# Kernel optimization log

Measured on AMD Instinct MI355X. Metric: run time of the kernel, lower is better.

## Reference

```python
import jax, jax.numpy as jnp
import numpy as np

D_MODEL = 512
N_HEAD = 8
D_HEAD = 64
N_LAYER = 4
D_INNER = 2048
IN_CH = 2048
N_CLS = 64
B, T = 2, 2048
LN_EPS = 1e-5


def layer_norm(x, s, b):
    mu = jnp.mean(x, axis=-1, keepdims=True)
    var = jnp.mean(jnp.square(x - mu), axis=-1, keepdims=True)
    return (x - mu) * jax.lax.rsqrt(var + LN_EPS) * s + b


def rel_shift(x):
    # x: [q, k, b, n] -> Transformer-XL relative shift
    q, k, b, n = x.shape
    zp = jnp.zeros((q, 1, b, n), x.dtype)
    x = jnp.concatenate([zp, x], axis=1)          # [q, k+1, b, n]
    x = x.reshape(k + 1, q, b, n)[1:]             # drop first row
    return x.reshape(q, k, b, n)


def setup_inputs() -> dict:
    key = jax.random.key(0)
    ks = jax.random.split(key, 12)
    s = 0.02
    return {
        "x": jax.random.normal(ks[0], (B, IN_CH, T), jnp.float32),
        "emb_w": jax.random.normal(ks[1], (D_MODEL, IN_CH), jnp.float32) * s,
        "emb_b": jnp.zeros((D_MODEL,), jnp.float32),
        "r_w_bias": jax.random.normal(ks[2], (N_HEAD, D_HEAD), jnp.float32) * s,
        "r_r_bias": jax.random.normal(ks[3], (N_HEAD, D_HEAD), jnp.float32) * s,
        "qkv_w": jax.random.normal(ks[4], (N_LAYER, 3 * N_HEAD * D_HEAD, D_MODEL), jnp.float32) * s,
        "qkv_b": jnp.zeros((N_LAYER, 3 * N_HEAD * D_HEAD), jnp.float32),
        "r_proj_w": jax.random.normal(ks[5], (N_LAYER, N_HEAD * D_HEAD, D_MODEL), jnp.float32) * s,
        "o_w": jax.random.normal(ks[6], (N_LAYER, D_MODEL, N_HEAD * D_HEAD), jnp.float32) * s,
        "ln1_s": jnp.ones((N_LAYER, D_MODEL), jnp.float32),
        "ln1_b": jnp.zeros((N_LAYER, D_MODEL), jnp.float32),
        "ff1_w": jax.random.normal(ks[7], (N_LAYER, D_INNER, D_MODEL), jnp.float32) * s,
        "ff1_b": jnp.zeros((N_LAYER, D_INNER), jnp.float32),
        "ff2_w": jax.random.normal(ks[8], (N_LAYER, D_MODEL, D_INNER), jnp.float32) * s,
        "ff2_b": jnp.zeros((N_LAYER, D_MODEL), jnp.float32),
        "ln2_s": jnp.ones((N_LAYER, D_MODEL), jnp.float32),
        "ln2_b": jnp.zeros((N_LAYER, D_MODEL), jnp.float32),
        "cls_w": jax.random.normal(ks[9], (N_CLS, D_MODEL), jnp.float32) * s,
        "cls_b": jnp.zeros((N_CLS,), jnp.float32),
    }


def reference(x, emb_w, emb_b, r_w_bias, r_r_bias, qkv_w, qkv_b, r_proj_w, o_w,
              ln1_s, ln1_b, ff1_w, ff1_b, ff2_w, ff2_b, ln2_s, ln2_b, cls_w, cls_b):
    b, _, t = x.shape
    d = D_MODEL
    # 1x1 conv embedding, then to [T, B, d_model] layout as in _forward
    h = jnp.einsum('dc,bct->tbd', emb_w, x) + emb_b

    # sinusoidal positional embedding over pos_seq = klen-1 .. 0 (klen == qlen, mem_len=0)
    pos_seq = jnp.arange(t - 1, -1, -1, dtype=h.dtype)
    inv_freq = 1.0 / (10000.0 ** (jnp.arange(0, d, 2, dtype=h.dtype) / d))
    sinusoid = pos_seq[:, None] * inv_freq[None, :]
    pos_emb = jnp.concatenate([jnp.sin(sinusoid), jnp.cos(sinusoid)], axis=-1)  # [T, d]

    scale = 1.0 / (D_HEAD ** 0.5)
    for i in range(N_LAYER):
        w = h
        heads = jnp.einsum('ed,tbd->tbe', qkv_w[i], w) + qkv_b[i]          # [T,B,3*H*Dh]
        q, k, v = jnp.split(heads, 3, axis=-1)
        q = q.reshape(t, b, N_HEAD, D_HEAD)
        k = k.reshape(t, b, N_HEAD, D_HEAD)
        v = v.reshape(t, b, N_HEAD, D_HEAD)
        r_head_k = jnp.einsum('ed,td->te', r_proj_w[i], pos_emb).reshape(t, N_HEAD, D_HEAD)

        AC = jnp.einsum('ibnd,jbnd->ijbn', q + r_w_bias, k)                # content term
        BD = rel_shift(jnp.einsum('ibnd,jnd->ijbn', q + r_r_bias, r_head_k))  # position term
        attn_prob = jax.nn.softmax((AC + BD) * scale, axis=1)              # softmax over keys
        attn_vec = jnp.einsum('ijbn,jbnd->ibnd', attn_prob, v).reshape(t, b, N_HEAD * D_HEAD)
        attn_out = jnp.einsum('de,tbe->tbd', o_w[i], attn_vec)             # o_net (no bias)
        h = layer_norm(w + attn_out, ln1_s[i], ln1_b[i])                   # post-lnorm

        ff = jnp.einsum('fd,tbd->tbf', ff1_w[i], h) + ff1_b[i]
        ff = jax.nn.relu(ff)
        ff = jnp.einsum('df,tbf->tbd', ff2_w[i], ff) + ff2_b[i]
        h = layer_norm(h + ff, ln2_s[i], ln2_b[i])

    # 1x1 conv classifier -> [B, num_classes, T]
    out = jnp.einsum('kd,tbd->bkt', cls_w, h) + cls_b[None, :, None]
    return out
```

## Files before the change

### kernel.cpp

```cpp
#include <hip/hip_runtime.h>
#include <hip/hip_bf16.h>
#include <math.h>


#define T_   2048
#define B_   2
#define DM   512
#define NH   8
#define DH   64
#define DI   2048
#define INCH 2048
#define NCLS 64
#define MT   4096

typedef __attribute__((ext_vector_type(8))) short short8;
typedef __attribute__((ext_vector_type(4))) float float4v;

#define QSCALE 0.1803368801111204f

__device__ inline ushort f2bf(float f) {
  uint u = __float_as_uint(f);
  return (ushort)((u + 0x7FFFu + ((u >> 16) & 1u)) >> 16);
}
__device__ inline float bf2f(ushort h) { return __uint_as_float(((uint)h) << 16); }
__device__ inline uint pkbf(float a, float b) {
  __hip_bfloat162 h = __float22bfloat162_rn(float2{a, b});
  return *(uint*)&h;
}
__device__ inline void gload16(const void* g, void* lds) {
  __builtin_amdgcn_global_load_lds(
      (const __attribute__((address_space(1))) void*)g,
      (__attribute__((address_space(3))) void*)lds, 16, 0, 0);
}

__global__ __launch_bounds__(256) void pos_kernel(ushort* __restrict__ pe) {
  int idx = blockIdx.x * 256 + threadIdx.x;
  if (idx >= T_ * DM) return;
  int t = idx >> 9;
  int i = idx & 511;
  int j = (i < 256) ? i : (i - 256);
  double invf = exp(-(double)(2 * j) * (9.210340371976184 / 512.0));
  double a = (double)(T_ - 1 - t) * invf;
  pe[idx] = f2bf((i < 256) ? (float)sin(a) : (float)cos(a));
}

__global__ __launch_bounds__(256) void cvt6_kernel(
    const float* s0, ushort* d0, int n0,
    const float* s1, ushort* d1, int n1,
    const float* s2, ushort* d2, int n2,
    const float* s3, ushort* d3, int n3,
    const float* s4, ushort* d4, int n4,
    const float* s5, ushort* d5, int n5)
{
  const float* s; ushort* d; int n;
  switch (blockIdx.y) {
    case 0: s = s0; d = d0; n = n0; break;
    case 1: s = s1; d = d1; n = n1; break;
    case 2: s = s2; d = d2; n = n2; break;
    case 3: s = s3; d = d3; n = n3; break;
    case 4: s = s4; d = d4; n = n4; break;
    default: s = s5; d = d5; n = n5; break;
  }
  int i = blockIdx.x * 256 + threadIdx.x;
  if (i >= n) return;
  float4 v = ((const float4*)s)[i];
  ushort4 w = { f2bf(v.x), f2bf(v.y), f2bf(v.z), f2bf(v.w) };
  ((ushort4*)d)[i] = w;
}

__global__ __launch_bounds__(256) void clsw_cvt_kernel(const float* __restrict__ w,
                                                       ushort* __restrict__ wb) {
  int i = blockIdx.x * 256 + threadIdx.x;
  ushort4 o;
  if (i < 8192) {
    float4 v = ((const float4*)w)[i];
    o = ushort4{ f2bf(v.x), f2bf(v.y), f2bf(v.z), f2bf(v.w) };
  } else {
    o = ushort4{ 0, 0, 0, 0 };
  }
  ((ushort4*)wb)[i] = o;
}

__global__ __launch_bounds__(256) void xpose_kernel(const float* __restrict__ x,
                                                    ushort* __restrict__ xb) {
  __shared__ float s[32][33];
  int t0 = blockIdx.x * 32, k0 = blockIdx.y * 32, b = blockIdx.z;
  int tx = threadIdx.x & 31, ty = threadIdx.x >> 5;
#pragma unroll
  for (int l = 0; l < 4; ++l) {
    int k = k0 + ty + l * 8;
    s[ty + l * 8][tx] = x[((size_t)b * INCH + k) * T_ + t0 + tx];
  }
  __syncthreads();
#pragma unroll
  for (int l = 0; l < 4; ++l) {
    int t = t0 + ty + l * 8;
    xb[((size_t)(t * 2 + b)) * INCH + k0 + tx] = f2bf(s[tx][ty + l * 8]);
  }
}

__global__ __launch_bounds__(256) void vtrans_kernel(const ushort* __restrict__ heads,
                                                     ushort* __restrict__ vtg) {
  __shared__ ushort s[64][72];
  const int tid = threadIdx.x;
  int t0 = blockIdx.x * 64;
  int b = blockIdx.y & 1, n = blockIdx.y >> 1;
  for (int e = tid; e < 512; e += 256) {
    int r = e >> 3, c = e & 7;
    *(uint4*)&s[r][c * 8] =
        *(const uint4*)&heads[(size_t)((t0 + r) * 2 + b) * 1536 + 1024 + n * 64 + c * 8];
  }
  __syncthreads();
  for (int e = tid; e < 512; e += 256) {
    int d = e >> 3, c = e & 7;
    ushort tmp[8];
#pragma unroll
    for (int j = 0; j < 8; ++j) tmp[j] = s[c * 8 + j][d];
    *(uint4*)&vtg[((size_t)((b * 8 + n) * 64 + d)) * (size_t)T_ + t0 + c * 8] = *(uint4*)tmp;
  }
}

template<int TM, int OUTMODE, bool RELU>
__global__ __launch_bounds__(256) void gemm_bf16(
    const ushort* __restrict__ A, const ushort* __restrict__ W,
    const float* __restrict__ bias, float* __restrict__ Cf, ushort* __restrict__ Cb,
    int M, int N, int K)
{
  __shared__ __attribute__((aligned(16))) ushort As[TM * 64];
  __shared__ __attribute__((aligned(16))) ushort Bs[128 * 64];
  const int NI = TM / 32;
  const int tid  = threadIdx.x;
  const int wave = tid >> 6, lane = tid & 63;
  const int quad = lane >> 4, lidx = lane & 15;
  const int m0 = blockIdx.y * TM, n0 = blockIdx.x * 128;
  const int r8 = lane >> 3;
  const int cs = ((lane & 7) ^ (r8 & 7)) * 8;

  float4v acc[NI * 4];
#pragma unroll
  for (int i = 0; i < NI * 4; ++i) acc[i] = (float4v){0.f, 0.f, 0.f, 0.f};

  const int wm = (wave >> 1) * (TM / 2), wn = (wave & 1) * 64;

  for (int k0 = 0; k0 < K; k0 += 64) {
    __syncthreads();
#pragma unroll
    for (int g = 0; g < TM / 32; ++g) {
      int r0 = wave * 8 + g * 32;
      gload16(A + (size_t)(m0 + r0 + r8) * K + k0 + cs, &As[r0 * 64]);
    }
#pragma unroll
    for (int g = 0; g < 4; ++g) {
      int r0 = wave * 8 + g * 32;
      gload16(W + (size_t)(n0 + r0 + r8) * K + k0 + cs, &Bs[r0 * 64]);
    }
    __syncthreads();

#pragma unroll
    for (int kb = 0; kb < 2; ++kb) {
      short8 af[NI], bf4[4];
      const int ch = (((kb * 4 + quad) ^ (lidx & 7)) * 8);
#pragma unroll
      for (int i = 0; i < NI; ++i)
        af[i] = *(const short8*)&As[(wm + i * 16 + lidx) * 64 + ch];
#pragma unroll
      for (int j = 0; j < 4; ++j)
        bf4[j] = *(const short8*)&Bs[(wn + j * 16 + lidx) * 64 + ch];
#pragma unroll
      for (int i = 0; i < NI; ++i)
#pragma unroll
        for (int j = 0; j < 4; ++j)
          acc[i * 4 + j] = __builtin_amdgcn_mfma_f32_16x16x32_bf16(af[i], bf4[j], acc[i * 4 + j], 0, 0, 0);
    }
  }

  float bj[4];
#pragma unroll
  for (int j = 0; j < 4; ++j) bj[j] = bias ? bias[n0 + wn + j * 16 + lidx] : 0.f;
#pragma unroll
  for (int i = 0; i < NI; ++i) {
    int rbase = m0 + wm + i * 16 + quad * 4;
#pragma unroll
    for (int j = 0; j < 4; ++j) {
      int col = n0 + wn + j * 16 + lidx;
#pragma unroll
      for (int reg = 0; reg < 4; ++reg) {
        float v = acc[i * 4 + j][reg] + bj[j];
        if (RELU) v = fmaxf(v, 0.f);
        size_t off = (size_t)(rbase + reg) * N + col;
        if (OUTMODE != 1) Cf[off] = v;
        if (OUTMODE != 0) Cb[off] = f2bf(v);
      }
    }
  }
}

#define GT 68

__device__ inline short8 bfrag(const char* base, int lidx, int quad, int kb) {
  return *(const short8*)(base + lidx * 128 + ((((kb << 2) + quad) ^ (lidx & 7)) << 4));
}

__global__ __launch_bounds__(256, 3) void attn_mfma_kernel(
    const ushort* __restrict__ heads, const ushort* __restrict__ rk,
    const ushort* __restrict__ vtg,
    const float* __restrict__ rwb, const float* __restrict__ rrb,
    float* __restrict__ O0, float* __restrict__ O1, float* __restrict__ O2,
    float* __restrict__ Lp)
{
  __shared__ __attribute__((aligned(16))) ushort Ks[64 * 64];
  __shared__ __attribute__((aligned(16))) ushort Vt[64 * 64];
  __shared__ __attribute__((aligned(16))) ushort Re[128 * 64];
  __shared__ __attribute__((aligned(16))) ushort Gbt[128 * GT];

  const int tid  = threadIdx.x;
  {
  }
  const int F = blockIdx.x + ((blockIdx.y + (blockIdx.z << 4)) << 5);
  const int g  = F & 7;
  const int k  = F >> 3;
  const int r  = k / 96;
  const int kk = k - r * 96;
  const int bnl = r * 8 + g;
  const int i0   = (kk & 31) * 64;
  const int chunk = kk >> 5;
  const int b    = bnl & 1;
  const int n    = bnl >> 1;
  const int jt0 = (chunk == 0) ? 0  : (chunk == 1 ? 11 : 22);
  const int jt1 = (chunk == 0) ? 11 : (chunk == 1 ? 22 : 32);
  const int wave = tid >> 6;
  const int lane = tid & 63;
  const int quad = lane >> 4;
  const int lidx = lane & 15;
  const int r8   = lane >> 3;
  const int cs8  = ((lane & 7) ^ (r8 & 7)) * 8;
  const int bn64 = (b * 8 + n) * 64;
  const int rloc = wave * 16 + lidx;

  short8 qw[2], qr4[4][2], q4[2];
  {
    auto qfrag = [&](int row, int kb, const float* bias) -> short8 {
      short8 q;
      if (row < T_) q = *(const short8*)&heads[(size_t)(row * 2 + b) * 1536 + n * 64 + kb * 32 + quad * 8];
      else { for (int t = 0; t < 8; ++t) ((ushort*)&q)[t] = 0; }
      short8 o;
#pragma unroll
      for (int t = 0; t < 8; ++t) {
        float f = (bf2f((ushort)((ushort*)&q)[t]) + bias[n * 64 + kb * 32 + quad * 8 + t]) * QSCALE;
        ((ushort*)&o)[t] = f2bf(f);
      }
      return o;
    };
    qw[0] = qfrag(i0 + rloc, 0, rwb);
    qw[1] = qfrag(i0 + rloc, 1, rwb);
#pragma unroll
    for (int rt = 0; rt < 4; ++rt) {
      int row = i0 + rt * 16 + lidx;
      qr4[rt][0] = qfrag(row, 0, rrb); qr4[rt][1] = qfrag(row, 1, rrb);
    }
    int row4 = i0 + 64 + lidx;
    q4[0] = qfrag(row4, 0, rrb); q4[1] = qfrag(row4, 1, rrb);
  }

  int a0[4];
#pragma unroll
  for (int t = 0; t < 4; ++t)
    a0[t] = (t * 16 + quad * 4 + 63 - rloc) * GT + rloc;

  float4v oacc[4];
  float4v liacc = (float4v){0.f, 0.f, 0.f, 0.f};
#pragma unroll
  for (int dt = 0; dt < 4; ++dt) oacc[dt] = (float4v){0.f, 0.f, 0.f, 0.f};
  short8 ones8;
#pragma unroll
  for (int t = 0; t < 8; ++t) ((ushort*)&ones8)[t] = 0x3F80;

  auto stageKRe = [&](int jt) {
    int j0 = jt * 64, qmin = j0 + 1984 - i0;
#pragma unroll
    for (int half = 0; half < 2; ++half) {
      int r0 = 8 * wave + 32 * half;
      gload16(heads + (size_t)((j0 + r0 + r8) * 2 + b) * 1536 + 512 + n * 64 + cs8, &Ks[r0 * 64]);
    }
#pragma unroll
    for (int q4i = 0; q4i < 4; ++q4i) {
      int r0 = 8 * wave + 32 * q4i;
      int qh = qmin + r0 + r8;
      int p  = (qh > T_) ? (qh - T_ - 1) : ((qh == T_) ? 0 : qh);
      gload16(rk + (size_t)p * 2048 + n * 64 + cs8, &Re[r0 * 64]);
    }
  };
  auto stageV = [&](int jt) {
    int j0 = jt * 64;
#pragma unroll
    for (int half = 0; half < 2; ++half) {
      int r0 = 8 * wave + 32 * half;
      gload16(vtg + (size_t)(bn64 + r0 + r8) * (size_t)T_ + j0 + cs8, &Vt[r0 * 64]);
    }
  };
  auto fixup = [&](int jt) {
    int qmin = jt * 64 + 1984 - i0;
    int Tidx = T_ - qmin;
    if (Tidx >= 0 && Tidx < 128) {
      if (tid < 32) ((uint*)Re)[Tidx * 32 + tid] = 0u;
      __syncthreads();
    }
  };

  stageKRe(jt0);
  stageV(jt0);
  __syncthreads();
  fixup(jt0);

  for (int jt = jt0; jt < jt1; ++jt) {
    const int qmin = jt * 64 + 1984 - i0;
    const int wth  = T_ - qmin;

    float4v sv[4];
#pragma unroll
    for (int t = 0; t < 4; ++t) {
      const char* KsT = (const char*)Ks + t * 2048;
      short8 kf0 = bfrag(KsT, lidx, quad, 0);
      short8 kf1 = bfrag(KsT, lidx, quad, 1);
      float4v c = {0.f, 0.f, 0.f, 0.f};
      c = __builtin_amdgcn_mfma_f32_16x16x32_bf16(kf0, qw[0], c, 0, 0, 0);
      c = __builtin_amdgcn_mfma_f32_16x16x32_bf16(kf1, qw[1], c, 0, 0, 0);
      sv[t] = c;
    }

#pragma unroll
    for (int si = 0; si < 2; ++si) {
      const int ws = wave + si * 4;
      const int w0 = ws * 16;
      const char* ReW = (const char*)Re + w0 * 128;
      short8 rb0 = bfrag(ReW, lidx, quad, 0);
      short8 rb1 = bfrag(ReW, lidx, quad, 1);
#pragma unroll
      for (int rt = 0; rt < 4; ++rt) {
        bool need = si == 0 ? (rt >= 3 - wave) : (rt <= 3 - wave);
        if (need) {
          float4v g2 = {0.f, 0.f, 0.f, 0.f};
          g2 = __builtin_amdgcn_mfma_f32_16x16x32_bf16(qr4[rt][0], rb0, g2, 0, 0, 0);
          g2 = __builtin_amdgcn_mfma_f32_16x16x32_bf16(qr4[rt][1], rb1, g2, 0, 0, 0);
          uint2 st; st.x = pkbf(g2[0], g2[1]); st.y = pkbf(g2[2], g2[3]);
          *(uint2*)&Gbt[(w0 + lidx) * GT + rt * 16 + quad * 4] = st;
        }
      }
      if (si == 0 && wth < 63) {
        float4v g2 = {0.f, 0.f, 0.f, 0.f};
        g2 = __builtin_amdgcn_mfma_f32_16x16x32_bf16(q4[0], rb0, g2, 0, 0, 0);
        g2 = __builtin_amdgcn_mfma_f32_16x16x32_bf16(q4[1], rb1, g2, 0, 0, 0);
        if (quad == 0) Gbt[(w0 + lidx) * GT + 64] = f2bf(g2[0]);
      }
    }
    __syncthreads();

    if (jt + 1 < jt1) stageKRe(jt + 1);

    if (wth >= 126) {
#pragma unroll
      for (int t = 0; t < 4; ++t)
#pragma unroll
        for (int r2 = 0; r2 < 4; ++r2)
          sv[t][r2] = __builtin_amdgcn_exp2f(sv[t][r2] + bf2f(Gbt[a0[t] + r2 * GT]));
    } else if (wth < 0) {
#pragma unroll
      for (int t = 0; t < 4; ++t)
#pragma unroll
        for (int r2 = 0; r2 < 4; ++r2)
          sv[t][r2] = __builtin_amdgcn_exp2f(sv[t][r2] + bf2f(Gbt[a0[t] + r2 * GT + 1]));
    } else {
      const int cth = wth + rloc - 63;
#pragma unroll
      for (int t = 0; t < 4; ++t) {
        const int c0 = t * 16 + quad * 4;
#pragma unroll
        for (int r2 = 0; r2 < 4; ++r2) {
          int ga = a0[t] + r2 * GT + ((c0 + r2 > cth) ? 1 : 0);
          sv[t][r2] = __builtin_amdgcn_exp2f(sv[t][r2] + bf2f(Gbt[ga]));
        }
      }
    }

    short8 vb[4][2];
#pragma unroll
    for (int dt = 0; dt < 4; ++dt) {
      const char* VtT = (const char*)Vt + dt * 2048;
      vb[dt][0] = bfrag(VtT, lidx, quad, 0);
      vb[dt][1] = bfrag(VtT, lidx, quad, 1);
    }

    short8 af[2];
#pragma unroll
    for (int kb = 0; kb < 2; ++kb) {
      uint mm[4];
#pragma unroll
      for (int i = 0; i < 2; ++i) {
        uint e, o;
        asm("v_cvt_pk_bf16_f32 %0, %1, %2" : "=v"(e) : "v"(sv[2 * kb][2 * i]),     "v"(sv[2 * kb][2 * i + 1]));
        asm("v_cvt_pk_bf16_f32 %0, %1, %2" : "=v"(o) : "v"(sv[2 * kb + 1][2 * i]), "v"(sv[2 * kb + 1][2 * i + 1]));
        asm("v_permlane32_swap_b32 %0, %1" : "+v"(e), "+v"(o));
        asm("v_permlane16_swap_b32 %0, %1" : "+v"(e), "+v"(o));
        mm[i] = e; mm[2 + i] = o;
      }
      union { uint u[4]; short8 s; } cv;
      cv.u[0] = mm[0]; cv.u[1] = mm[1]; cv.u[2] = mm[2]; cv.u[3] = mm[3];
      af[kb] = cv.s;
    }

#pragma unroll
    for (int dt = 0; dt < 4; ++dt) {
      oacc[dt] = __builtin_amdgcn_mfma_f32_16x16x32_bf16(af[0], vb[dt][0], oacc[dt], 0, 0, 0);
      oacc[dt] = __builtin_amdgcn_mfma_f32_16x16x32_bf16(af[1], vb[dt][1], oacc[dt], 0, 0, 0);
    }
    liacc = __builtin_amdgcn_mfma_f32_16x16x32_bf16(af[0], ones8, liacc, 0, 0, 0);
    liacc = __builtin_amdgcn_mfma_f32_16x16x32_bf16(af[1], ones8, liacc, 0, 0, 0);

    __syncthreads();

    if (jt + 1 < jt1) {
      stageV(jt + 1);
      fixup(jt + 1);
    }
  }

  float* __restrict__ Oc = (chunk == 0) ? O0 : (chunk == 1 ? O1 : O2);
  float* __restrict__ Lc = Lp + chunk * (16 * T_);
  const int rowg0 = (b * 8 + n) * T_ + i0 + wave * 16 + quad * 4;
#pragma unroll
  for (int reg = 0; reg < 4; ++reg) {
    int rowg = rowg0 + reg;
#pragma unroll
    for (int dt = 0; dt < 4; ++dt)
      Oc[(size_t)rowg * 64 + dt * 16 + lidx] = oacc[dt][reg];
    if (lidx == 0) Lc[rowg] = liacc[reg];
  }
}

__global__ __launch_bounds__(256) void attn_norm_kernel(
    const float* __restrict__ O0, const float* __restrict__ O1,
    const float* __restrict__ O2, const float* __restrict__ Lp,
    ushort* __restrict__ avec)
{
  int idx = blockIdx.x * 256 + threadIdx.x;
  int d4  = idx & 15;
  int row = (idx >> 4) & 2047;
  int bn  = idx >> 15;
  float4 v0 = ((const float4*)O0)[idx];
  float4 v1 = ((const float4*)O1)[idx];
  float4 v2 = ((const float4*)O2)[idx];
  int rg = (bn << 11) + row;
  float li = Lp[rg] + Lp[rg + 16 * T_] + Lp[rg + 32 * T_];
  float inv = 1.0f / li;
  int b = bn >> 3, n = bn & 7;
  ushort4 w = { f2bf((v0.x + v1.x + v2.x) * inv), f2bf((v0.y + v1.y + v2.y) * inv),
                f2bf((v0.z + v1.z + v2.z) * inv), f2bf((v0.w + v1.w + v2.w) * inv) };
  *(ushort4*)&avec[(size_t)(row * 2 + b) * DM + n * 64 + d4 * 4] = w;
}

__global__ __launch_bounds__(256) void ln_res_kernel(
    float* __restrict__ h, ushort* __restrict__ hb, const float* __restrict__ delta,
    const float* __restrict__ s, const float* __restrict__ bb)
{
  const int m = blockIdx.x;
  const int tid = threadIdx.x;
  float* hp = h + (size_t)m * DM;
  ushort* hbp = hb + (size_t)m * DM;
  const float* dp = delta + (size_t)m * DM;
  float x0 = hp[tid] + dp[tid];
  float x1 = hp[tid + 256] + dp[tid + 256];
  float sum = x0 + x1, sq = x0 * x0 + x1 * x1;
#pragma unroll
  for (int o = 32; o > 0; o >>= 1) { sum += __shfl_down(sum, o); sq += __shfl_down(sq, o); }
  __shared__ float part[8];
  int wv = tid >> 6;
  if ((tid & 63) == 0) { part[wv * 2] = sum; part[wv * 2 + 1] = sq; }
  __syncthreads();
  float ts = part[0] + part[2] + part[4] + part[6];
  float tq = part[1] + part[3] + part[5] + part[7];
  float mu = ts * (1.f / DM);
  float var = tq * (1.f / DM) - mu * mu;
  float rs = rsqrtf(var + 1e-5f);
  float y0 = (x0 - mu) * rs * s[tid]       + bb[tid];
  float y1 = (x1 - mu) * rs * s[tid + 256] + bb[tid + 256];
  hp[tid] = y0;       hbp[tid] = f2bf(y0);
  hp[tid + 256] = y1; hbp[tid + 256] = f2bf(y1);
}

__global__ __launch_bounds__(256) void reorder_kernel(const float* __restrict__ ct,
                                                      const float* __restrict__ cb,
                                                      float* __restrict__ out) {
  int idx = blockIdx.x * 256 + threadIdx.x;
  if (idx >= B_ * NCLS * T_) return;
  int t  = idx & (T_ - 1);
  int nc = (idx >> 11) & 63;
  int bb = idx >> 17;
  out[idx] = ct[(size_t)(t * B_ + bb) * 128 + nc] + cb[nc];
}

extern "C" void kernel_launch(void* const* d_in, const int* in_sizes, int n_in,
                              void* d_out, int out_size, void* d_ws, size_t ws_size,
                              hipStream_t stream)
{
  const float* x     = (const float*)d_in[0];
  const float* emb_w = (const float*)d_in[1];
  const float* emb_b = (const float*)d_in[2];
  const float* rwb   = (const float*)d_in[3];
  const float* rrb   = (const float*)d_in[4];
  const float* qkv_w = (const float*)d_in[5];
  const float* qkv_b = (const float*)d_in[6];
  const float* rproj = (const float*)d_in[7];
  const float* o_w   = (const float*)d_in[8];
  const float* ln1s  = (const float*)d_in[9];
  const float* ln1b  = (const float*)d_in[10];
  const float* ff1w  = (const float*)d_in[11];
  const float* ff1b  = (const float*)d_in[12];
  const float* ff2w  = (const float*)d_in[13];
  const float* ff2b  = (const float*)d_in[14];
  const float* ln2s  = (const float*)d_in[15];
  const float* ln2b  = (const float*)d_in[16];
  const float* clsw  = (const float*)d_in[17];
  const float* clsb  = (const float*)d_in[18];
  float* out = (float*)d_out;

  char* p = (char*)d_ws;
  float*  h       = (float*)p;   p += (size_t)MT * DM * 4;
  float*  tmpf    = (float*)p;   p += (size_t)MT * DM * 4;
  ushort* hb      = (ushort*)p;  p += (size_t)MT * DM * 2;
  ushort* headsb  = (ushort*)p;  p += (size_t)MT * 1536 * 2;
  ushort* peb     = (ushort*)p;  p += (size_t)T_ * DM * 2;
  ushort* rk_all  = (ushort*)p;  p += (size_t)T_ * 2048 * 2;
  ushort* avecb   = (ushort*)p;  p += (size_t)MT * DM * 2;
  ushort* xfb     = (ushort*)p;  p += (size_t)MT * INCH * 2;
  ushort* emb_wb  = (ushort*)p;  p += (size_t)DM * INCH * 2;
  ushort* qkv_wb  = (ushort*)p;  p += (size_t)4 * 1536 * DM * 2;
  ushort* rproj_wb= (ushort*)p;  p += (size_t)4 * DM * DM * 2;
  ushort* o_wb    = (ushort*)p;  p += (size_t)4 * DM * DM * 2;
  ushort* ff1_wb  = (ushort*)p;  p += (size_t)4 * DI * DM * 2;
  ushort* ff2_wb  = (ushort*)p;  p += (size_t)4 * DM * DI * 2;
  float*  P2      = (float*)p;   p += (size_t)MT * DM * 4;
  float*  Lp      = (float*)p;   p += (size_t)3 * 16 * T_ * 4;
  ushort* cls_wb  = (ushort*)p;  p += (size_t)128 * DM * 2;
  ushort* vtg     = xfb;
  float*  P0      = tmpf;
  float*  P1      = (float*)(xfb + (size_t)16 * 64 * T_);

  cvt6_kernel<<<dim3(4096, 6), 256, 0, stream>>>(
      emb_w, emb_wb, DM * INCH / 4,
      qkv_w, qkv_wb, 4 * 1536 * DM / 4,
      rproj, rproj_wb, 4 * DM * DM / 4,
      o_w,   o_wb,   4 * DM * DM / 4,
      ff1w,  ff1_wb, 4 * DI * DM / 4,
      ff2w,  ff2_wb, 4 * DM * DI / 4);
  clsw_cvt_kernel<<<64, 256, 0, stream>>>(clsw, cls_wb);
  pos_kernel<<<(T_ * DM) / 256, 256, 0, stream>>>(peb);
  xpose_kernel<<<dim3(T_ / 32, INCH / 32, B_), 256, 0, stream>>>(x, xfb);

  gemm_bf16<64, 2, false><<<dim3(DM / 128, MT / 64), 256, 0, stream>>>(
      xfb, emb_wb, emb_b, h, hb, MT, DM, INCH);
  gemm_bf16<128, 1, false><<<dim3(2048 / 128, T_ / 128), 256, 0, stream>>>(
      peb, rproj_wb, nullptr, nullptr, rk_all, T_, 2048, DM);

  for (int l = 0; l < 4; ++l) {
    gemm_bf16<128, 1, false><<<dim3(1536 / 128, MT / 128), 256, 0, stream>>>(
        hb, qkv_wb + (size_t)l * 1536 * DM, qkv_b + l * 1536, nullptr, headsb, MT, 1536, DM);
    vtrans_kernel<<<dim3(T_ / 64, B_ * NH), 256, 0, stream>>>(headsb, vtg);
    attn_mfma_kernel<<<dim3(T_ / 64, B_ * NH, 3), 256, 0, stream>>>(
        headsb, rk_all + (size_t)l * 512, vtg, rwb, rrb, P0, P1, P2, Lp);
    attn_norm_kernel<<<(16 * T_ * 16) / 256, 256, 0, stream>>>(P0, P1, P2, Lp, avecb);
    gemm_bf16<32, 0, false><<<dim3(DM / 128, MT / 32), 256, 0, stream>>>(
        avecb, o_wb + (size_t)l * DM * DM, nullptr, tmpf, nullptr, MT, DM, DM);
    ln_res_kernel<<<MT, 256, 0, stream>>>(h, hb, tmpf, ln1s + l * DM, ln1b + l * DM);
    gemm_bf16<128, 1, true><<<dim3(DI / 128, MT / 128), 256, 0, stream>>>(
        hb, ff1_wb + (size_t)l * DI * DM, ff1b + l * DI, nullptr, xfb, MT, DI, DM);
    gemm_bf16<32, 0, false><<<dim3(DM / 128, MT / 32), 256, 0, stream>>>(
        xfb, ff2_wb + (size_t)l * DM * DI, ff2b + l * DM, tmpf, nullptr, MT, DM, DI);
    ln_res_kernel<<<MT, 256, 0, stream>>>(h, hb, tmpf, ln2s + l * DM, ln2b + l * DM);
  }

  gemm_bf16<32, 0, false><<<dim3(1, MT / 32), 256, 0, stream>>>(
      hb, cls_wb, nullptr, tmpf, nullptr, MT, 128, DM);
  reorder_kernel<<<(B_ * NCLS * T_) / 256, 256, 0, stream>>>(tmpf, clsb, out);
}
```

Before: 832.1 us.

## Load K and V fragments directly from global memory, drop LDS staging

The attention kernel stops staging K and V tiles through shared memory. Each wave now reads its MFMA fragments for K and V straight from global memory into registers, which frees LDS and allows raising the occupancy hint from 3 to 4 blocks per CU. This removes the LDS writes and reads for K and V. In exchange, every wave issues redundant uncoalesced-ish global loads for the same tiles, and those loads are no longer prefetched ahead of use, so global latency sits on the critical path.

Result: slower. 1.234 ms (+48.3%).

```diff
diff --git a/kernel.cpp b/kernel.cpp
--- a/kernel.cpp
+++ b/kernel.cpp
@@ -201,21 +201,17 @@
   return *(const short8*)(base + lidx * 128 + ((((kb << 2) + quad) ^ (lidx & 7)) << 4));
 }
 
-__global__ __launch_bounds__(256, 3) void attn_mfma_kernel(
+__global__ __launch_bounds__(256, 4) void attn_mfma_kernel(
     const ushort* __restrict__ heads, const ushort* __restrict__ rk,
     const ushort* __restrict__ vtg,
     const float* __restrict__ rwb, const float* __restrict__ rrb,
     float* __restrict__ O0, float* __restrict__ O1, float* __restrict__ O2,
     float* __restrict__ Lp)
 {
-  __shared__ __attribute__((aligned(16))) ushort Ks[64 * 64];
-  __shared__ __attribute__((aligned(16))) ushort Vt[64 * 64];
   __shared__ __attribute__((aligned(16))) ushort Re[128 * 64];
   __shared__ __attribute__((aligned(16))) ushort Gbt[128 * GT];
 
   const int tid  = threadIdx.x;
-  {
-  }
   const int F = blockIdx.x + ((blockIdx.y + (blockIdx.z << 4)) << 5);
   const int g  = F & 7;
   const int k  = F >> 3;
@@ -237,6 +233,9 @@
   const int bn64 = (b * 8 + n) * 64;
   const int rloc = wave * 16 + lidx;
 
+  const ushort* kbase = heads + (size_t)(lidx * 2 + b) * 1536 + 512 + n * 64 + quad * 8;
+  const ushort* vbase = vtg + (size_t)(bn64 + lidx) * (size_t)T_ + quad * 8;
+
   short8 qw[2], qr4[4][2], q4[2];
   {
     auto qfrag = [&](int row, int kb, const float* bias) -> short8 {
@@ -275,27 +274,14 @@
 #pragma unroll
   for (int t = 0; t < 8; ++t) ((ushort*)&ones8)[t] = 0x3F80;
 
-  auto stageKRe = [&](int jt) {
-    int j0 = jt * 64, qmin = j0 + 1984 - i0;
-#pragma unroll
-    for (int half = 0; half < 2; ++half) {
-      int r0 = 8 * wave + 32 * half;
-      gload16(heads + (size_t)((j0 + r0 + r8) * 2 + b) * 1536 + 512 + n * 64 + cs8, &Ks[r0 * 64]);
-    }
+  auto stageRe = [&](int jt) {
+    int qmin = jt * 64 + 1984 - i0;
 #pragma unroll
     for (int q4i = 0; q4i < 4; ++q4i) {
       int r0 = 8 * wave + 32 * q4i;
       int qh = qmin + r0 + r8;
       int p  = (qh > T_) ? (qh - T_ - 1) : ((qh == T_) ? 0 : qh);
       gload16(rk + (size_t)p * 2048 + n * 64 + cs8, &Re[r0 * 64]);
-    }
-  };
-  auto stageV = [&](int jt) {
-    int j0 = jt * 64;
-#pragma unroll
-    for (int half = 0; half < 2; ++half) {
-      int r0 = 8 * wave + 32 * half;
-      gload16(vtg + (size_t)(bn64 + r0 + r8) * (size_t)T_ + j0 + cs8, &Vt[r0 * 64]);
     }
   };
   auto fixup = [&](int jt) {
@@ -307,24 +293,29 @@
     }
   };
 
-  stageKRe(jt0);
-  stageV(jt0);
+  stageRe(jt0);
   __syncthreads();
   fixup(jt0);
 
   for (int jt = jt0; jt < jt1; ++jt) {
-    const int qmin = jt * 64 + 1984 - i0;
+    const int j0   = jt * 64;
+    const int qmin = j0 + 1984 - i0;
     const int wth  = T_ - qmin;
 
+    short8 kf[4][2];
+#pragma unroll
+    for (int t = 0; t < 4; ++t) {
+      const ushort* kp = kbase + (size_t)(j0 + t * 16) * 3072;
+      kf[t][0] = *(const short8*)(kp);
+      kf[t][1] = *(const short8*)(kp + 32);
+    }
+
     float4v sv[4];
 #pragma unroll
     for (int t = 0; t < 4; ++t) {
-      const char* KsT = (const char*)Ks + t * 2048;
-      short8 kf0 = bfrag(KsT, lidx, quad, 0);
-      short8 kf1 = bfrag(KsT, lidx, quad, 1);
       float4v c = {0.f, 0.f, 0.f, 0.f};
-      c = __builtin_amdgcn_mfma_f32_16x16x32_bf16(kf0, qw[0], c, 0, 0, 0);
-      c = __builtin_amdgcn_mfma_f32_16x16x32_bf16(kf1, qw[1], c, 0, 0, 0);
+      c = __builtin_amdgcn_mfma_f32_16x16x32_bf16(kf[t][0], qw[0], c, 0, 0, 0);
+      c = __builtin_amdgcn_mfma_f32_16x16x32_bf16(kf[t][1], qw[1], c, 0, 0, 0);
       sv[t] = c;
     }
 
@@ -355,7 +346,7 @@
     }
     __syncthreads();
 
-    if (jt + 1 < jt1) stageKRe(jt + 1);
+    if (jt + 1 < jt1) stageRe(jt + 1);
 
     if (wth >= 126) {
 #pragma unroll
@@ -385,9 +376,9 @@
     short8 vb[4][2];
 #pragma unroll
     for (int dt = 0; dt < 4; ++dt) {
-      const char* VtT = (const char*)Vt + dt * 2048;
-      vb[dt][0] = bfrag(VtT, lidx, quad, 0);
-      vb[dt][1] = bfrag(VtT, lidx, quad, 1);
+      const ushort* vp = vbase + (size_t)dt * 16 * T_ + j0;
+      vb[dt][0] = *(const short8*)(vp);
+      vb[dt][1] = *(const short8*)(vp + 32);
     }
 
     short8 af[2];
@@ -418,10 +409,7 @@
 
     __syncthreads();
 
-    if (jt + 1 < jt1) {
-      stageV(jt + 1);
-      fixup(jt + 1);
-    }
+    if (jt + 1 < jt1) fixup(jt + 1);
   }
 
   float* __restrict__ Oc = (chunk == 0) ? O0 : (chunk == 1 ? O1 : O2);
```
